# Kernel tuning notes

Hardware: AMD Instinct MI355X
Metric: run time of the kernel (lower is better)

## Reference

```python
import jax, jax.numpy as jnp
import numpy as np

N_GRAPHS = 1024  # number of disjoint graphs for global_mean_pool


def gcn_conv(x, src, dst, W, b, n):
    h = x @ W  # [N, out]
    deg = jax.ops.segment_sum(jnp.ones_like(dst, dtype=h.dtype), dst, num_segments=n) + 1.0  # +1 self loop
    dinv = jax.lax.rsqrt(deg)  # [N]
    coef = dinv[src] * dinv[dst]  # [E]
    agg = jax.ops.segment_sum(h[src] * coef[:, None], dst, num_segments=n)
    agg = agg + h * (dinv * dinv)[:, None]  # self-loop contribution
    return agg + b


def setup_inputs() -> dict:
    key = jax.random.key(0)
    ks = jax.random.split(key, 9)
    N, E, F_IN, H, D = 50000, 800000, 128, 256, 768
    x = jax.random.normal(ks[0], (N, F_IN), dtype=jnp.float32)
    edge_index = jax.random.randint(ks[1], (2, E), 0, N)
    batch = jnp.sort(jax.random.randint(ks[2], (N,), 0, N_GRAPHS))
    s = lambda k, sh, fan: jax.random.normal(k, sh, jnp.float32) * (1.0 / np.sqrt(fan))
    return dict(
        x=x, edge_index=edge_index, batch=batch,
        W1=s(ks[3], (F_IN, H), F_IN), b1=jnp.zeros((H,), jnp.float32),
        W2=s(ks[4], (H, H), H), b2=jnp.zeros((H,), jnp.float32),
        W3=s(ks[5], (H, H), H), b3=jnp.zeros((H,), jnp.float32),
        P1=s(ks[6], (H, H), H), pb1=jnp.zeros((H,), jnp.float32),
        P2=s(ks[7], (H, D), H), pb2=jnp.zeros((D,), jnp.float32),
        ln_g=jnp.ones((D,), jnp.float32), ln_b=jnp.zeros((D,), jnp.float32),
    )


def reference(x, edge_index, batch, W1, b1, W2, b2, W3, b3, P1, pb1, P2, pb2, ln_g, ln_b):
    n = x.shape[0]
    src, dst = edge_index[0], edge_index[1]
    h1 = jax.nn.relu(gcn_conv(x, src, dst, W1, b1, n))
    h2 = jax.nn.relu(gcn_conv(h1, src, dst, W2, b2, n)) + h1
    h3 = jax.nn.relu(gcn_conv(h2, src, dst, W3, b3, n)) + h2
    # global_mean_pool
    sums = jax.ops.segment_sum(h3, batch, num_segments=N_GRAPHS)
    cnt = jax.ops.segment_sum(jnp.ones((n,), h3.dtype), batch, num_segments=N_GRAPHS)
    g = sums / jnp.maximum(cnt, 1.0)[:, None]  # [G, 256]
    # projection MLP (dropout is identity in eval)
    g = jax.nn.relu(g @ P1 + pb1) @ P2 + pb2  # [G, D]
    # LayerNorm
    mu = jnp.mean(g, axis=-1, keepdims=True)
    var = jnp.mean((g - mu) ** 2, axis=-1, keepdims=True)
    return (g - mu) * jax.lax.rsqrt(var + 1e-5) * ln_g + ln_b
```

## Files before the change

### kernel.cpp

```cpp
#include <hip/hip_runtime.h>


typedef __attribute__((ext_vector_type(8))) short short8;
typedef __attribute__((ext_vector_type(4))) float f32x4;
typedef __attribute__((ext_vector_type(2))) float f32x2;

__device__ __forceinline__ float bf2f(unsigned short s) {
    union { unsigned u; float f; } v;
    v.u = ((unsigned)s) << 16;
    return v.f;
}
__device__ __forceinline__ unsigned short f2bf(float f) {
    union { float f; unsigned u; } v;
    v.f = f;
    unsigned r = (v.u + 0x7FFFu + ((v.u >> 16) & 1u)) >> 16;
    return (unsigned short)r;
}
__device__ __forceinline__ unsigned pk2bf(float lo, float hi) {
    return (unsigned)f2bf(lo) | ((unsigned)f2bf(hi) << 16);
}
__device__ __forceinline__ unsigned short u4c(ushort4 v, int p) {
    return p == 0 ? v.x : p == 1 ? v.y : p == 2 ? v.z : v.w;
}

__device__ __forceinline__ void acc8_fp8(unsigned int lo, unsigned int hi, f32x2* acc2) {
    acc2[0] += __builtin_amdgcn_cvt_pk_f32_fp8(lo, false);
    acc2[1] += __builtin_amdgcn_cvt_pk_f32_fp8(lo, true);
    acc2[2] += __builtin_amdgcn_cvt_pk_f32_fp8(hi, false);
    acc2[3] += __builtin_amdgcn_cvt_pk_f32_fp8(hi, true);
}


__global__ void count_wt(const int* __restrict__ dst, int E,
                         int* __restrict__ cnt, int* __restrict__ rank,
                         const float* __restrict__ W1, const float* __restrict__ W2,
                         const float* __restrict__ W3, const float* __restrict__ P1,
                         const float* __restrict__ P2,
                         unsigned short* __restrict__ Wt1, unsigned short* __restrict__ Wt2,
                         unsigned short* __restrict__ Wt3, unsigned short* __restrict__ Pt1,
                         unsigned short* __restrict__ Pt2,
                         int F_IN, int H, int D,
                         unsigned char* __restrict__ zx,
                         unsigned char* __restrict__ z1,
                         unsigned char* __restrict__ z2) {
    int gidx = blockIdx.x * blockDim.x + threadIdx.x;
    if (gidx < E) {
        rank[gidx] = atomicAdd(&cnt[dst[gidx]], 1);
        return;
    }
    int t = gidx - E;
    int n1 = F_IN * H, n2 = H * H, n5 = H * D;
    const float* W; unsigned short* O; int Nn, kshift;
    if (t < n1)              { W = W1; O = Wt1; Nn = H; kshift = 7; }
    else if ((t -= n1) < n2) { W = W2; O = Wt2; Nn = H; kshift = 8; }
    else if ((t -= n2) < n2) { W = W3; O = Wt3; Nn = H; kshift = 8; }
    else if ((t -= n2) < n2) { W = P1; O = Pt1; Nn = H; kshift = 8; }
    else if ((t -= n2) < n5) { W = P2; O = Pt2; Nn = D; kshift = 8; }
    else {
        t -= n5;
        if (t < 128) zx[t] = 0;
        else if (t < 384) z1[t - 128] = 0;
        else if (t < 640) z2[t - 384] = 0;
        return;
    }
    int n = t >> kshift, k = t & ((1 << kshift) - 1);
    O[t] = f2bf(W[(size_t)k * Nn + n]);
}

__global__ void scanA(const int* __restrict__ cnt, int n, int* __restrict__ bsum,
                      float* __restrict__ dinv) {
    int tid = threadIdx.x, lane = tid & 63, w = tid >> 6;
    int i = blockIdx.x * 512 + tid;
    int v = (i < n) ? cnt[i] : 0;
    if (i < n) dinv[i] = rsqrtf((float)v + 1.0f);
    int s = v;
    #pragma unroll
    for (int off = 1; off < 64; off <<= 1) s += __shfl_xor(s, off);
    __shared__ int ws[8];
    if (lane == 0) ws[w] = s;
    __syncthreads();
    if (tid == 0) {
        int t = 0;
        #pragma unroll
        for (int j = 0; j < 8; j++) t += ws[j];
        bsum[blockIdx.x] = t;
    }
}

__global__ void scanC(const int* __restrict__ cnt, int n, const int* __restrict__ bsum,
                      int E, int* __restrict__ row_ptr) {
    int tid = threadIdx.x, lane = tid & 63, w = tid >> 6;
    int i = blockIdx.x * 512 + tid;
    __shared__ int s_boff;
    if (tid < 64) {
        int acc = 0;
        for (int b = tid; b < blockIdx.x; b += 64) acc += bsum[b];
        #pragma unroll
        for (int off = 1; off < 64; off <<= 1) acc += __shfl_xor(acc, off);
        if (tid == 0) s_boff = acc;
    }
    int v = (i < n) ? cnt[i] : 0;
    int incl = v;
    #pragma unroll
    for (int off = 1; off < 64; off <<= 1) {
        int t = __shfl_up(incl, off);
        if (lane >= off) incl += t;
    }
    __shared__ int ws[8];
    if (lane == 63) ws[w] = incl;
    __syncthreads();
    int woff = 0;
    for (int j = 0; j < w; j++) woff += ws[j];
    if (i < n) row_ptr[i] = s_boff + woff + incl - v;
    if (blockIdx.x == 0 && tid == 0) row_ptr[n] = E;
}

__global__ void scatter_x(const int* __restrict__ src, const int* __restrict__ dst,
                          const int* __restrict__ row_ptr, const int* __restrict__ rank,
                          int* __restrict__ csr, int E,
                          const float* __restrict__ x, const float* __restrict__ dinv,
                          unsigned char* __restrict__ xf8, int n4) {
    int gidx = blockIdx.x * blockDim.x + threadIdx.x;
    if (gidx < E) {
        csr[row_ptr[dst[gidx]] + rank[gidx]] = src[gidx];
        return;
    }
    int idx = gidx - E;
    if (idx < n4) {
        float di = dinv[idx >> 5];
        float4 v = ((const float4*)x)[idx];
        unsigned int p = 0;
        p = __builtin_amdgcn_cvt_pk_fp8_f32(di * v.x, di * v.y, p, false);
        p = __builtin_amdgcn_cvt_pk_fp8_f32(di * v.z, di * v.w, p, true);
        ((unsigned int*)xf8)[idx] = p;
    }
}


__launch_bounds__(256, 8)
__global__ void aggregate256(const unsigned char* __restrict__ hf8,
                             const int* __restrict__ row_ptr,
                             const int* __restrict__ csr,
                             unsigned short* __restrict__ out, int n, int zrow) {
    int node = blockIdx.x * 4 + (threadIdx.x >> 6);
    int lane = threadIdx.x & 63;
    if (node >= n) return;
    int half = lane >> 5;
    int cl = lane & 31;
    f32x2 acc2[4];
    #pragma unroll
    for (int c = 0; c < 4; c++) acc2[c] = (f32x2){0.f, 0.f};
    if (half == 0) {
        uint2 sv = *(const uint2*)(hf8 + ((unsigned)node * 256u + (unsigned)cl * 8u));
        acc8_fp8(sv.x, sv.y, acc2);
    }
    int beg = row_ptr[node], end = row_ptr[node + 1];
    for (int base = beg; base < end; base += 64) {
        int k = base + lane;
        int mi = (k < end) ? csr[k] : zrow;
        int cnt = min(64, end - base);
        for (int j = 0; j < cnt; j += 16) {
            unsigned off[8]; uint2 vv[8];
            #pragma unroll
            for (int u = 0; u < 8; u++)
                off[u] = (unsigned)__shfl(mi, j + 2 * u + half) * 256u + (unsigned)cl * 8u;
            #pragma unroll
            for (int u = 0; u < 8; u++) vv[u] = *(const uint2*)(hf8 + off[u]);
            #pragma unroll
            for (int u = 0; u < 8; u++) acc8_fp8(vv[u].x, vv[u].y, acc2);
        }
    }
    #pragma unroll
    for (int c = 0; c < 4; c++) {
        acc2[c][0] += __shfl_xor(acc2[c][0], 32);
        acc2[c][1] += __shfl_xor(acc2[c][1], 32);
    }
    if (half == 0) {
        short8 o;
        #pragma unroll
        for (int c = 0; c < 8; c++) o[c] = (short)f2bf(acc2[c >> 1][c & 1]);
        *(short8*)(out + (size_t)node * 256 + cl * 8) = o;
    }
}

__launch_bounds__(256, 8)
__global__ void aggregate128(const unsigned char* __restrict__ hf8,
                             const int* __restrict__ row_ptr,
                             const int* __restrict__ csr,
                             unsigned short* __restrict__ out, int n, int zrow) {
    int node = blockIdx.x * 4 + (threadIdx.x >> 6);
    int lane = threadIdx.x & 63;
    if (node >= n) return;
    int qtr = lane >> 4;
    int cl = lane & 15;
    f32x2 acc2[4];
    #pragma unroll
    for (int c = 0; c < 4; c++) acc2[c] = (f32x2){0.f, 0.f};
    if (qtr == 0) {
        uint2 sv = *(const uint2*)(hf8 + ((unsigned)node * 128u + (unsigned)cl * 8u));
        acc8_fp8(sv.x, sv.y, acc2);
    }
    int beg = row_ptr[node], end = row_ptr[node + 1];
    for (int base = beg; base < end; base += 64) {
        int k = base + lane;
        int mi = (k < end) ? csr[k] : zrow;
        int cnt = min(64, end - base);
        for (int j = 0; j < cnt; j += 32) {
            unsigned off[8]; uint2 vv[8];
            #pragma unroll
            for (int u = 0; u < 8; u++)
                off[u] = (unsigned)__shfl(mi, j + 4 * u + qtr) * 128u + (unsigned)cl * 8u;
            #pragma unroll
            for (int u = 0; u < 8; u++) vv[u] = *(const uint2*)(hf8 + off[u]);
            #pragma unroll
            for (int u = 0; u < 8; u++) acc8_fp8(vv[u].x, vv[u].y, acc2);
        }
    }
    #pragma unroll
    for (int c = 0; c < 4; c++) {
        acc2[c][0] += __shfl_xor(acc2[c][0], 16);
        acc2[c][1] += __shfl_xor(acc2[c][1], 16);
        acc2[c][0] += __shfl_xor(acc2[c][0], 32);
        acc2[c][1] += __shfl_xor(acc2[c][1], 32);
    }
    if (qtr == 0) {
        short8 o;
        #pragma unroll
        for (int c = 0; c < 8; c++) o[c] = (short)f2bf(acc2[c >> 1][c & 1]);
        *(short8*)(out + (size_t)node * 128 + cl * 8) = o;
    }
}


template<int K, int RELU, int RES, int OUTF32, int SCALE, int FP8O>
__launch_bounds__(256)
__global__ void wgemm(const unsigned short* __restrict__ A,
                      const unsigned short* __restrict__ Bt,
                      const float* __restrict__ bias,
                      const unsigned short* __restrict__ residual,
                      const float* __restrict__ dinv,
                      void* __restrict__ Cout,
                      unsigned char* __restrict__ f8out,
                      int M, int N, int ntiles) {
    constexpr int KK = K / 32;
    constexpr int CPR = K / 8;
    __shared__ __align__(16) unsigned short Bs[64 * K];

    int tid = threadIdx.x;
    int wave = tid >> 6, lane = tid & 63;
    int r = lane & 15, q = lane >> 4;
    int mr = blockIdx.y * 128 + wave * 32;
    int nbase = blockIdx.x * ntiles * 64;

    short8 a[2][KK];
    #pragma unroll
    for (int mi = 0; mi < 2; mi++) {
        int arow = mr + mi * 16 + r;
        bool aok = arow < M;
        const unsigned short* ap = A + (size_t)(aok ? arow : 0) * K;
        #pragma unroll
        for (int kk = 0; kk < KK; kk++) {
            short8 v = *(const short8*)(ap + kk * 32 + q * 8);
            if (!aok) v = (short8){0, 0, 0, 0, 0, 0, 0, 0};
            a[mi][kk] = v;
        }
    }

    for (int t = 0; t < ntiles; t++) {
        int n0 = nbase + t * 64;
        if (t > 0) __syncthreads();
        #pragma unroll
        for (int pass = 0; pass < 64 * CPR / 256; pass++) {
            int f = pass * 256 + tid;
            int row = f / CPR, ch = f % CPR;
            *(short8*)&Bs[row * K + (ch ^ (row & 7)) * 8] =
                *(const short8*)(Bt + (size_t)(n0 + row) * K + ch * 8);
        }
        __syncthreads();

        f32x4 acc[2][4];
        #pragma unroll
        for (int mi = 0; mi < 2; mi++)
            #pragma unroll
            for (int j = 0; j < 4; j++) acc[mi][j] = (f32x4){0.f, 0.f, 0.f, 0.f};

        #pragma unroll
        for (int kk = 0; kk < KK; kk++) {
            short8 b[4];
            #pragma unroll
            for (int j = 0; j < 4; j++)
                b[j] = *(short8*)&Bs[(j * 16 + r) * K + ((kk * 4 + q) ^ (r & 7)) * 8];
            #pragma unroll
            for (int mi = 0; mi < 2; mi++)
                #pragma unroll
                for (int j = 0; j < 4; j++)
                    acc[mi][j] = __builtin_amdgcn_mfma_f32_16x16x32_bf16(b[j], a[mi][kk], acc[mi][j], 0, 0, 0);
        }

        f32x4 bq[4];
        #pragma unroll
        for (int j = 0; j < 4; j++)
            bq[j] = *(const f32x4*)&bias[n0 + j * 16 + q * 4];

        #pragma unroll
        for (int mi = 0; mi < 2; mi++) {
            int m = mr + mi * 16 + r;
            bool ok = m < M;
            float di = 1.f, rdi = 1.f;
            if (SCALE) { di = dinv[ok ? m : 0]; if (RES) rdi = 1.f / di; }
            ushort4 rv[4];
            if (RES) {
                const unsigned short* rp = residual + (size_t)(ok ? m : 0) * N + n0 + q * 4;
                #pragma unroll
                for (int j = 0; j < 4; j++) rv[j] = *(const ushort4*)(rp + j * 16);
            }
            float u[4][4];
            #pragma unroll
            for (int j = 0; j < 4; j++)
                #pragma unroll
                for (int p = 0; p < 4; p++) {
                    float v = (SCALE ? di * acc[mi][j][p] : acc[mi][j][p]) + bq[j][p];
                    if (RELU) v = fmaxf(v, 0.f);
                    if (RES) v += bf2f(u4c(rv[j], p)) * rdi;
                    if (SCALE == 1) v *= di;
                    u[j][p] = v;
                }

            if (OUTF32) {
                float c4[4][4], tf[4][4];
                #pragma unroll
                for (int j = 0; j < 4; j++)
                    #pragma unroll
                    for (int d = 0; d < 4; d++) c4[j][d] = u[j][d];
                #pragma unroll
                for (int j = 0; j < 4; j++)
                    #pragma unroll
                    for (int d = 0; d < 4; d++) tf[j][d] = __shfl_xor(c4[j ^ 1][d], 16);
                #pragma unroll
                for (int j = 0; j < 4; j++)
                    #pragma unroll
                    for (int d = 0; d < 4; d++)
                        c4[j][d] = (((j ^ q) & 1) == 0) ? c4[j][d] : tf[j][d];
                #pragma unroll
                for (int j = 0; j < 4; j++)
                    #pragma unroll
                    for (int d = 0; d < 4; d++) tf[j][d] = __shfl_xor(c4[j ^ 2][d], 32);
                #pragma unroll
                for (int j = 0; j < 4; j++)
                    #pragma unroll
                    for (int d = 0; d < 4; d++)
                        c4[j][d] = (((j ^ q) & 2) == 0) ? c4[j][d] : tf[j][d];
                if (ok) {
                    float* cp = (float*)Cout + (size_t)m * N + n0 + q * 16;
                    #pragma unroll
                    for (int j = 0; j < 4; j++) *(f32x4*)&cp[j * 4] = *(f32x4*)&c4[j][0];
                }
            } else {
                unsigned db[4][2], tb[4][2];
                #pragma unroll
                for (int j = 0; j < 4; j++) {
                    db[j][0] = pk2bf(u[j][0], u[j][1]);
                    db[j][1] = pk2bf(u[j][2], u[j][3]);
                }
                #pragma unroll
                for (int j = 0; j < 4; j++)
                    #pragma unroll
                    for (int d = 0; d < 2; d++) tb[j][d] = __shfl_xor((int)db[j ^ 1][d], 16);
                #pragma unroll
                for (int j = 0; j < 4; j++)
                    #pragma unroll
                    for (int d = 0; d < 2; d++)
                        db[j][d] = (((j ^ q) & 1) == 0) ? db[j][d] : tb[j][d];
                #pragma unroll
                for (int j = 0; j < 4; j++)
                    #pragma unroll
                    for (int d = 0; d < 2; d++) tb[j][d] = __shfl_xor((int)db[j ^ 2][d], 32);
                #pragma unroll
                for (int j = 0; j < 4; j++)
                    #pragma unroll
                    for (int d = 0; d < 2; d++)
                        db[j][d] = (((j ^ q) & 2) == 0) ? db[j][d] : tb[j][d];
                if (ok) {
                    unsigned short* cp = (unsigned short*)Cout + (size_t)m * N + n0 + q * 16;
                    *(uint4*)cp = make_uint4(db[0][0], db[0][1], db[1][0], db[1][1]);
                    *(uint4*)(cp + 8) = make_uint4(db[2][0], db[2][1], db[3][0], db[3][1]);
                }
                if (FP8O) {
                    unsigned f8[4], t8[4];
                    #pragma unroll
                    for (int j = 0; j < 4; j++) {
                        unsigned p8 = 0;
                        p8 = __builtin_amdgcn_cvt_pk_fp8_f32(u[j][0], u[j][1], p8, false);
                        p8 = __builtin_amdgcn_cvt_pk_fp8_f32(u[j][2], u[j][3], p8, true);
                        f8[j] = p8;
                    }
                    #pragma unroll
                    for (int j = 0; j < 4; j++) t8[j] = __shfl_xor((int)f8[j ^ 1], 16);
                    #pragma unroll
                    for (int j = 0; j < 4; j++)
                        f8[j] = (((j ^ q) & 1) == 0) ? f8[j] : t8[j];
                    #pragma unroll
                    for (int j = 0; j < 4; j++) t8[j] = __shfl_xor((int)f8[j ^ 2], 32);
                    #pragma unroll
                    for (int j = 0; j < 4; j++)
                        f8[j] = (((j ^ q) & 2) == 0) ? f8[j] : t8[j];
                    if (ok) {
                        unsigned char* fp = f8out + (size_t)m * N + n0 + q * 16;
                        *(uint4*)fp = make_uint4(f8[0], f8[1], f8[2], f8[3]);
                    }
                }
            }
        }
    }
}


__launch_bounds__(256)
__global__ void pool_kernel(const unsigned short* __restrict__ h, const int* __restrict__ batch,
                            unsigned short* __restrict__ g0, int n, int G) {
    int g = blockIdx.x * 4 + (threadIdx.x >> 6);
    int lane = threadIdx.x & 63;
    if (g >= G) return;
    int a = 0, b = n;
    while (a < b) { int m = (a + b) >> 1; if (batch[m] < g) a = m + 1; else b = m; }
    int lo = a;
    int a2 = a, b2 = n;
    while (a2 < b2) { int m = (a2 + b2) >> 1; if (batch[m] < g + 1) a2 = m + 1; else b2 = m; }
    int hi = a2;
    float s[4][4];
    #pragma unroll
    for (int u = 0; u < 4; u++)
        #pragma unroll
        for (int c = 0; c < 4; c++) s[u][c] = 0.f;
    int i = lo;
    for (; i + 4 <= hi; i += 4) {
        ushort4 v[4];
        #pragma unroll
        for (int u = 0; u < 4; u++)
            v[u] = *(const ushort4*)(h + (size_t)(i + u) * 256 + lane * 4);
        #pragma unroll
        for (int u = 0; u < 4; u++) {
            s[u][0] += bf2f(v[u].x); s[u][1] += bf2f(v[u].y);
            s[u][2] += bf2f(v[u].z); s[u][3] += bf2f(v[u].w);
        }
    }
    for (; i < hi; i++) {
        ushort4 v = *(const ushort4*)(h + (size_t)i * 256 + lane * 4);
        s[0][0] += bf2f(v.x); s[0][1] += bf2f(v.y);
        s[0][2] += bf2f(v.z); s[0][3] += bf2f(v.w);
    }
    float a0 = s[0][0] + s[1][0] + s[2][0] + s[3][0];
    float a1 = s[0][1] + s[1][1] + s[2][1] + s[3][1];
    float a2f = s[0][2] + s[1][2] + s[2][2] + s[3][2];
    float a3 = s[0][3] + s[1][3] + s[2][3] + s[3][3];
    float inv = 1.0f / fmaxf((float)(hi - lo), 1.0f);
    ushort4 o;
    o.x = f2bf(a0 * inv); o.y = f2bf(a1 * inv); o.z = f2bf(a2f * inv); o.w = f2bf(a3 * inv);
    *(ushort4*)(g0 + (size_t)g * 256 + lane * 4) = o;
}

__launch_bounds__(256)
__global__ void ln_kernel(const float* __restrict__ g2, const float* __restrict__ gamma,
                          const float* __restrict__ beta, float* __restrict__ out, int rows) {
    int row = blockIdx.x * 4 + (threadIdx.x >> 6);
    int lane = threadIdx.x & 63;
    if (row >= rows) return;
    const float* r = g2 + (size_t)row * 768;
    float v[12];
    float s = 0.f, s2 = 0.f;
    #pragma unroll
    for (int j = 0; j < 12; j++) {
        v[j] = r[lane + 64 * j];
        s += v[j];
        s2 += v[j] * v[j];
    }
    #pragma unroll
    for (int off = 32; off > 0; off >>= 1) {
        s += __shfl_down(s, off);
        s2 += __shfl_down(s2, off);
    }
    s = __shfl(s, 0);
    s2 = __shfl(s2, 0);
    float mu = s * (1.0f / 768.0f);
    float var = s2 * (1.0f / 768.0f) - mu * mu;
    float inv = rsqrtf(var + 1e-5f);
    #pragma unroll
    for (int j = 0; j < 12; j++) {
        int c = lane + 64 * j;
        out[(size_t)row * 768 + c] = (v[j] - mu) * inv * gamma[c] + beta[c];
    }
}


extern "C" void kernel_launch(void* const* d_in, const int* in_sizes, int n_in,
                              void* d_out, int out_size, void* d_ws, size_t ws_size,
                              hipStream_t stream) {
    const float* x    = (const float*)d_in[0];
    const int* eidx   = (const int*)d_in[1];
    const int* batch  = (const int*)d_in[2];
    const float* W1   = (const float*)d_in[3];
    const float* b1   = (const float*)d_in[4];
    const float* W2   = (const float*)d_in[5];
    const float* b2   = (const float*)d_in[6];
    const float* W3   = (const float*)d_in[7];
    const float* b3   = (const float*)d_in[8];
    const float* P1   = (const float*)d_in[9];
    const float* pb1  = (const float*)d_in[10];
    const float* P2   = (const float*)d_in[11];
    const float* pb2  = (const float*)d_in[12];
    const float* ln_g = (const float*)d_in[13];
    const float* ln_b = (const float*)d_in[14];
    float* out = (float*)d_out;

    const int N = in_sizes[2];
    const int E = in_sizes[1] / 2;
    const int F_IN = in_sizes[0] / N;
    const int H = in_sizes[4];
    const int D = in_sizes[12];
    const int G = out_size / D;
    const int NPAD = (N + 127) & ~127;
    const int NB = (N + 511) / 512;

    const int* src = eidx;
    const int* dst = eidx + E;

    char* ws = (char*)d_ws;
    size_t off = 0;
    auto alloc = [&](size_t bytes) -> char* {
        char* p = ws + off;
        off = (off + bytes + 255) & ~(size_t)255;
        return p;
    };
    int*   cnt      = (int*)alloc((size_t)NPAD * 4);
    float* dinv     = (float*)alloc((size_t)NPAD * 4);
    int*   row_ptr  = (int*)alloc((size_t)(N + 1) * 4);
    int*   bsum     = (int*)alloc(128 * 4);
    int*   rank     = (int*)alloc((size_t)E * 4);
    int*   csr      = (int*)alloc((size_t)E * 4);
    unsigned char* xf8  = (unsigned char*)alloc((size_t)(N + 1) * F_IN);
    unsigned char* h1f8 = (unsigned char*)alloc((size_t)(N + 1) * H);
    unsigned char* h2f8 = (unsigned char*)alloc((size_t)(N + 1) * H);
    unsigned short* Wt1 = (unsigned short*)alloc((size_t)F_IN * H * 2);
    unsigned short* Wt2 = (unsigned short*)alloc((size_t)H * H * 2);
    unsigned short* Wt3 = (unsigned short*)alloc((size_t)H * H * 2);
    unsigned short* Pt1 = (unsigned short*)alloc((size_t)H * H * 2);
    unsigned short* Pt2 = (unsigned short*)alloc((size_t)H * D * 2);
    unsigned short* t1  = (unsigned short*)alloc((size_t)N * F_IN * 2);
    unsigned short* tA  = (unsigned short*)alloc((size_t)N * H * 2);
    unsigned short* hh1 = (unsigned short*)alloc((size_t)N * H * 2);
    unsigned short* hh2 = (unsigned short*)alloc((size_t)N * H * 2);
    unsigned short* h3  = (unsigned short*)alloc((size_t)N * H * 2);
    unsigned short* g0b = (unsigned short*)alloc((size_t)G * H * 2);
    unsigned short* g1b = (unsigned short*)alloc((size_t)G * H * 2);
    float* g2 = (float*)alloc((size_t)G * D * 4);
    (void)ws_size; (void)n_in;

    hipMemsetAsync(cnt, 0, (size_t)NPAD * 4, stream);
    {
        int tot = F_IN * H + 3 * H * H + H * D;
        int total = E + tot + 640;
        count_wt<<<(total + 255) / 256, 256, 0, stream>>>(
            dst, E, cnt, rank, W1, W2, W3, P1, P2, Wt1, Wt2, Wt3, Pt1, Pt2,
            F_IN, H, D,
            xf8 + (size_t)N * F_IN, h1f8 + (size_t)N * H, h2f8 + (size_t)N * H);
    }
    scanA<<<NB, 512, 0, stream>>>(cnt, N, bsum, dinv);
    scanC<<<NB, 512, 0, stream>>>(cnt, N, bsum, E, row_ptr);

    {
        int n4 = N * F_IN / 4;
        scatter_x<<<(E + n4 + 255) / 256, 256, 0, stream>>>(
            src, dst, row_ptr, rank, csr, E, x, dinv, xf8, n4);
    }

    int agg_grid = (N + 3) / 4;
    int mtiles = (N + 127) / 128;

    aggregate128<<<agg_grid, 256, 0, stream>>>(xf8, row_ptr, csr, t1, N, N);
    wgemm<128, 1, 0, 0, 1, 1><<<dim3(2, mtiles), 256, 0, stream>>>(t1, Wt1, b1, nullptr, dinv, hh1, h1f8, N, H, 2);

    aggregate256<<<agg_grid, 256, 0, stream>>>(h1f8, row_ptr, csr, tA, N, N);
    wgemm<256, 1, 1, 0, 1, 1><<<dim3(2, mtiles), 256, 0, stream>>>(tA, Wt2, b2, hh1, dinv, hh2, h2f8, N, H, 2);

    aggregate256<<<agg_grid, 256, 0, stream>>>(h2f8, row_ptr, csr, tA, N, N);
    wgemm<256, 1, 1, 0, 2, 0><<<dim3(2, mtiles), 256, 0, stream>>>(tA, Wt3, b3, hh2, dinv, h3, nullptr, N, H, 2);

    pool_kernel<<<(G + 3) / 4, 256, 0, stream>>>(h3, batch, g0b, N, G);
    wgemm<256, 1, 0, 0, 0, 0><<<dim3(4, G / 128), 256, 0, stream>>>(g0b, Pt1, pb1, nullptr, nullptr, g1b, nullptr, G, H, 1);
    wgemm<256, 0, 0, 1, 0, 0><<<dim3(12, G / 128), 256, 0, stream>>>(g1b, Pt2, pb2, nullptr, nullptr, g2, nullptr, G, D, 1);
    ln_kernel<<<G / 4, 256, 0, stream>>>(g2, ln_g, ln_b, out, G);
}
```

Before: 343.9 us.

## Build CSR with atomic cursors instead of per-edge rank array

The degree-count pass no longer records a per-edge rank. It reads dst four at a time and only increments counts. The scan now also writes a cursor array seeded with row_ptr, and the scatter pass claims CSR slots with atomicAdd on that cursor. This removes the E-sized rank write and read, at the cost of atomics in the scatter and a nondeterministic neighbour order within each row, which can change floating-point summation order.

```diff
diff --git a/kernel.cpp b/kernel.cpp
--- a/kernel.cpp
+++ b/kernel.cpp
@@ -31,8 +31,8 @@
 }
 
 
-__global__ void count_wt(const int* __restrict__ dst, int E,
-                         int* __restrict__ cnt, int* __restrict__ rank,
+__global__ void count_wt(const int* __restrict__ dst, int E, int nE4, int rem,
+                         int* __restrict__ cnt,
                          const float* __restrict__ W1, const float* __restrict__ W2,
                          const float* __restrict__ W3, const float* __restrict__ P1,
                          const float* __restrict__ P2,
@@ -44,11 +44,20 @@
                          unsigned char* __restrict__ z1,
                          unsigned char* __restrict__ z2) {
     int gidx = blockIdx.x * blockDim.x + threadIdx.x;
-    if (gidx < E) {
-        rank[gidx] = atomicAdd(&cnt[dst[gidx]], 1);
+    if (gidx < nE4) {
+        uint4 d4 = *(const uint4*)(dst + 4 * gidx);
+        atomicAdd(&cnt[d4.x], 1);
+        atomicAdd(&cnt[d4.y], 1);
+        atomicAdd(&cnt[d4.z], 1);
+        atomicAdd(&cnt[d4.w], 1);
         return;
     }
-    int t = gidx - E;
+    int t = gidx - nE4;
+    if (t < rem) {
+        atomicAdd(&cnt[dst[4 * nE4 + t]], 1);
+        return;
+    }
+    t -= rem;
     int n1 = F_IN * H, n2 = H * H, n5 = H * D;
     const float* W; unsigned short* O; int Nn, kshift;
     if (t < n1)              { W = W1; O = Wt1; Nn = H; kshift = 7; }
@@ -88,7 +97,7 @@
 }
 
 __global__ void scanC(const int* __restrict__ cnt, int n, const int* __restrict__ bsum,
-                      int E, int* __restrict__ row_ptr) {
+                      int E, int* __restrict__ row_ptr, int* __restrict__ cursor) {
     int tid = threadIdx.x, lane = tid & 63, w = tid >> 6;
     int i = blockIdx.x * 512 + tid;
     __shared__ int s_boff;
@@ -111,18 +120,23 @@
     __syncthreads();
     int woff = 0;
     for (int j = 0; j < w; j++) woff += ws[j];
-    if (i < n) row_ptr[i] = s_boff + woff + incl - v;
+    if (i < n) {
+        int rp = s_boff + woff + incl - v;
+        row_ptr[i] = rp;
+        cursor[i] = rp;
+    }
     if (blockIdx.x == 0 && tid == 0) row_ptr[n] = E;
 }
 
 __global__ void scatter_x(const int* __restrict__ src, const int* __restrict__ dst,
-                          const int* __restrict__ row_ptr, const int* __restrict__ rank,
+                          int* __restrict__ cursor,
                           int* __restrict__ csr, int E,
                           const float* __restrict__ x, const float* __restrict__ dinv,
                           unsigned char* __restrict__ xf8, int n4) {
     int gidx = blockIdx.x * blockDim.x + threadIdx.x;
     if (gidx < E) {
-        csr[row_ptr[dst[gidx]] + rank[gidx]] = src[gidx];
+        int slot = atomicAdd(&cursor[dst[gidx]], 1);
+        csr[slot] = src[gidx];
         return;
     }
     int idx = gidx - E;
@@ -535,7 +549,7 @@
     float* dinv     = (float*)alloc((size_t)NPAD * 4);
     int*   row_ptr  = (int*)alloc((size_t)(N + 1) * 4);
     int*   bsum     = (int*)alloc(128 * 4);
-    int*   rank     = (int*)alloc((size_t)E * 4);
+    int*   cursor   = (int*)alloc((size_t)(N + 1) * 4);
     int*   csr      = (int*)alloc((size_t)E * 4);
     unsigned char* xf8  = (unsigned char*)alloc((size_t)(N + 1) * F_IN);
     unsigned char* h1f8 = (unsigned char*)alloc((size_t)(N + 1) * H);
@@ -557,20 +571,21 @@
 
     hipMemsetAsync(cnt, 0, (size_t)NPAD * 4, stream);
     {
+        int nE4 = E >> 2, rem = E & 3;
         int tot = F_IN * H + 3 * H * H + H * D;
-        int total = E + tot + 640;
+        int total = nE4 + rem + tot + 640;
         count_wt<<<(total + 255) / 256, 256, 0, stream>>>(
-            dst, E, cnt, rank, W1, W2, W3, P1, P2, Wt1, Wt2, Wt3, Pt1, Pt2,
+            dst, E, nE4, rem, cnt, W1, W2, W3, P1, P2, Wt1, Wt2, Wt3, Pt1, Pt2,
             F_IN, H, D,
             xf8 + (size_t)N * F_IN, h1f8 + (size_t)N * H, h2f8 + (size_t)N * H);
     }
     scanA<<<NB, 512, 0, stream>>>(cnt, N, bsum, dinv);
-    scanC<<<NB, 512, 0, stream>>>(cnt, N, bsum, E, row_ptr);
+    scanC<<<NB, 512, 0, stream>>>(cnt, N, bsum, E, row_ptr, cursor);
 
     {
         int n4 = N * F_IN / 4;
         scatter_x<<<(E + n4 + 255) / 256, 256, 0, stream>>>(
-            src, dst, row_ptr, rank, csr, E, x, dinv, xf8, n4);
+            src, dst, cursor, csr, E, x, dinv, xf8, n4);
     }
 
     int agg_grid = (N + 3) / 4;
```

Result: slower. 375.6 us (+9.2%).
